# Performance work log

Measured on AMD Instinct MI355X. Metric: run time of the kernel, lower is better.

## Reference

```python
import jax, jax.numpy as jnp
import numpy as np

D_MODEL = 1024
NUM_HEADS = 16
D_K = D_MODEL // NUM_HEADS


def setup_inputs() -> dict:
    key = jax.random.key(0)
    ks = jax.random.split(key, 12)
    B, S = 2, 2048
    s = 1.0 / np.sqrt(D_MODEL)
    inp = {
        "query": jax.random.normal(ks[0], (B, S, D_MODEL), jnp.float32),
        "key": jax.random.normal(ks[1], (B, S, D_MODEL), jnp.float32),
        "value": jax.random.normal(ks[2], (B, S, D_MODEL), jnp.float32),
        "w_q": jax.random.normal(ks[3], (D_MODEL, D_MODEL), jnp.float32) * s,
        "b_q": jax.random.normal(ks[4], (D_MODEL,), jnp.float32) * 0.01,
        "w_k": jax.random.normal(ks[5], (D_MODEL, D_MODEL), jnp.float32) * s,
        "b_k": jax.random.normal(ks[6], (D_MODEL,), jnp.float32) * 0.01,
        "w_v": jax.random.normal(ks[7], (D_MODEL, D_MODEL), jnp.float32) * s,
        "b_v": jax.random.normal(ks[8], (D_MODEL,), jnp.float32) * 0.01,
        "w_o": jax.random.normal(ks[9], (D_MODEL, D_MODEL), jnp.float32) * s,
        "b_o": jax.random.normal(ks[10], (D_MODEL,), jnp.float32) * 0.01,
    }
    return inp


def _split_heads(x):
    # [B, S, d_model] -> [B, H, S, d_k]
    B, S, _ = x.shape
    return x.reshape(B, S, NUM_HEADS, D_K).transpose(0, 2, 1, 3)


def reference(query, key, value, w_q, b_q, w_k, b_k, w_v, b_v, w_o, b_o):
    B, S, _ = query.shape
    Q = _split_heads(query @ w_q.T + b_q)
    K = _split_heads(key @ w_k.T + b_k)
    V = _split_heads(value @ w_v.T + b_v)
    scale = 1.0 / jnp.sqrt(jnp.asarray(D_K, Q.dtype))
    scores = jnp.einsum("bhqd,bhkd->bhqk", Q, K) * scale  # [B,H,S,S]
    attn = jax.nn.softmax(scores, axis=-1)
    ctx = jnp.einsum("bhqk,bhkd->bhqd", attn, V)
    ctx = ctx.transpose(0, 2, 1, 3).reshape(B, S, D_MODEL)
    return ctx @ w_o.T + b_o
```

## Files before the change

### kernel.cpp

```cpp
#include <hip/hip_runtime.h>
#include <hip/hip_bf16.h>
#include <stdint.h>

#define D_MODEL 1024
#define NHEAD   16
#define DK      64
#define SEQ     2048
#define BATCH   2

using bf16 = __bf16;
typedef __bf16 bf16x8 __attribute__((ext_vector_type(8)));
typedef float  f32x4  __attribute__((ext_vector_type(4)));
typedef float  f32x16 __attribute__((ext_vector_type(16)));
typedef unsigned uintx2 __attribute__((ext_vector_type(2)));

__device__ __forceinline__ unsigned short f2bf(float x) {
  return __builtin_bit_cast(unsigned short, (__bf16)x);
}
__device__ __forceinline__ unsigned pk2bf(float a, float b) {
  return (unsigned)f2bf(a) | ((unsigned)f2bf(b) << 16);
}
__device__ __forceinline__ float uasf(unsigned x) {
  return __builtin_bit_cast(float, x);
}
__device__ __forceinline__ unsigned fasu(float x) {
  return __builtin_bit_cast(unsigned, x);
}

__device__ __forceinline__ void gld_lds16(const void* g, void* l) {
  __builtin_amdgcn_global_load_lds(
      (const __attribute__((address_space(1))) void*)g,
      (__attribute__((address_space(3))) void*)l, 16, 0, 0);
}

__device__ __forceinline__ float xhalf_sum(float x) {
  uintx2 r = __builtin_amdgcn_permlane32_swap(fasu(x), fasu(x), false, false);
  return uasf(r[0]) + uasf(r[1]);
}

#define MHA_PACK(sv, off, dst)                                           \
  {                                                                      \
    float e0 = __builtin_amdgcn_exp2f(sv[off + 0]);                      \
    float e1 = __builtin_amdgcn_exp2f(sv[off + 1]);                      \
    float e2 = __builtin_amdgcn_exp2f(sv[off + 2]);                      \
    float e3 = __builtin_amdgcn_exp2f(sv[off + 3]);                      \
    float e4 = __builtin_amdgcn_exp2f(sv[off + 4]);                      \
    float e5 = __builtin_amdgcn_exp2f(sv[off + 5]);                      \
    float e6 = __builtin_amdgcn_exp2f(sv[off + 6]);                      \
    float e7 = __builtin_amdgcn_exp2f(sv[off + 7]);                      \
    ps += ((e0 + e1) + (e2 + e3)) + ((e4 + e5) + (e6 + e7));             \
    unsigned c0 = pk2bf(e0, e1), c1 = pk2bf(e2, e3);                     \
    unsigned c2 = pk2bf(e4, e5), c3 = pk2bf(e6, e7);                     \
    uintx2 r02 = __builtin_amdgcn_permlane32_swap(c0, c2, false, false); \
    uintx2 r13 = __builtin_amdgcn_permlane32_swap(c1, c3, false, false); \
    uint4 w; w.x = r02[0]; w.y = r13[0]; w.z = r02[1]; w.w = r13[1];     \
    dst = __builtin_bit_cast(bf16x8, w);                                 \
  }

struct ConvArgs {
  const float* src[7];
  bf16* dst[7];
};

__global__ __launch_bounds__(256) void convert_f32_bf16(ConvArgs a) {
  int v = blockIdx.x * 256 + threadIdx.x;
  int seg, off;
  if (v < 3 * 1048576) { seg = v >> 20; off = v & (1048576 - 1); }
  else { int u = v - 3 * 1048576; seg = 3 + (u >> 18); off = u & (262144 - 1); }
  float4 f = ((const float4*)a.src[seg])[off];
  ushort4 o;
  o.x = f2bf(f.x); o.y = f2bf(f.y); o.z = f2bf(f.z); o.w = f2bf(f.w);
  ((ushort4*)a.dst[seg])[off] = o;
}

__device__ __forceinline__ void gemm_qkv_core(
    const bf16* __restrict__ A, const bf16* __restrict__ B,
    const float* __restrict__ bias, bf16* __restrict__ Cout,
    int mode, int bx, int by, float oscale, char* lds) {
  constexpr int BUF = 16384;
  constexpr int NKT = D_MODEL / 32;
  const int tid  = threadIdx.x;
  const int lane = tid & 63;
  const int wave = tid >> 6;
  const int wr = wave >> 1, wc = wave & 1;
  const int t = lane >> 4, q = lane & 15;

  f32x4 acc[4][4];
#pragma unroll
  for (int i = 0; i < 4; ++i)
#pragma unroll
    for (int j = 0; j < 4; ++j) acc[i][j] = (f32x4){0.f, 0.f, 0.f, 0.f};

  const char* Abase = (const char*)(A + (size_t)bx * 128 * D_MODEL);
  const char* Bbase = (const char*)(B + (size_t)by * 128 * D_MODEL);

  const char* gA[2]; char* sA[2]; const char* gB[2]; char* sB[2];
#pragma unroll
  for (int i = 0; i < 2; ++i) {
    int c = tid + i * 256, row = c >> 2;
    int src = ((c & 3) * 16) ^ ((row & 3) << 4);
    gA[i] = Abase + (size_t)row * (D_MODEL * 2) + src;
    sA[i] = lds + c * 16;
    gB[i] = Bbase + (size_t)row * (D_MODEL * 2) + src;
    sB[i] = lds + 8192 + c * 16;
  }

  const char* aA[4]; const char* aB[4];
#pragma unroll
  for (int f = 0; f < 4; ++f) {
    int ra = wr * 64 + f * 16 + q;
    aA[f] = lds + ra * 64 + ((t * 16) ^ ((q & 3) << 4));
    int rb = wc * 64 + f * 16 + q;
    aB[f] = lds + 8192 + rb * 64 + ((t * 16) ^ ((q & 3) << 4));
  }

#pragma unroll
  for (int i = 0; i < 2; ++i) { gld_lds16(gA[i], sA[i]); gld_lds16(gB[i], sB[i]); }
#pragma unroll
  for (int i = 0; i < 2; ++i) {
    gld_lds16(gA[i] + 64, sA[i] + BUF); gld_lds16(gB[i] + 64, sB[i] + BUF);
  }
  asm volatile("s_waitcnt vmcnt(4)" ::: "memory");
  __builtin_amdgcn_s_barrier();

#pragma unroll
  for (int kt = 0; kt < NKT; ++kt) {
    const int CUR = (kt % 3) * BUF;
    if (kt + 2 < NKT) {
      const int NB = ((kt + 2) % 3) * BUF;
#pragma unroll
      for (int i = 0; i < 2; ++i) {
        gld_lds16(gA[i] + (kt + 2) * 64, sA[i] + NB);
        gld_lds16(gB[i] + (kt + 2) * 64, sB[i] + NB);
      }
    }
    bf16x8 af[4], bfv[4];
#pragma unroll
    for (int f = 0; f < 4; ++f) af[f]  = *(const bf16x8*)(aA[f] + CUR);
#pragma unroll
    for (int f = 0; f < 4; ++f) bfv[f] = *(const bf16x8*)(aB[f] + CUR);
    __builtin_amdgcn_s_setprio(1);
#pragma unroll
    for (int fm = 0; fm < 4; ++fm)
#pragma unroll
      for (int fn = 0; fn < 4; ++fn)
        acc[fm][fn] = __builtin_amdgcn_mfma_f32_16x16x32_bf16(
            af[fm], bfv[fn], acc[fm][fn], 0, 0, 0);
    __builtin_amdgcn_s_setprio(0);
    if (kt + 2 < NKT)      asm volatile("s_waitcnt vmcnt(4)" ::: "memory");
    else if (kt + 1 < NKT) asm volatile("s_waitcnt vmcnt(0)" ::: "memory");
    __builtin_amdgcn_s_barrier();
  }

#pragma unroll
  for (int fm = 0; fm < 4; ++fm)
#pragma unroll
    for (int fn = 0; fn < 4; ++fn)
#pragma unroll
      for (int jj = 0; jj < 4; ++jj) {
        int m = bx * 128 + wr * 64 + fm * 16 + t * 4 + jj;
        int n = by * 128 + wc * 64 + fn * 16 + q;
        float v = acc[fm][fn][jj];
        if (mode == 0) {
          v = (v + bias[n]) * oscale;
          int b = m >> 11, s = m & (SEQ - 1), h = n >> 6, d = n & 63;
          Cout[(((size_t)(b * NHEAD + h)) * SEQ + s) * DK + d] = (bf16)v;
        } else {
          v += bias[m];
          int h = m >> 6, d = m & 63, b = n >> 11, s = n & (SEQ - 1);
          Cout[(((size_t)(b * NHEAD + h)) * DK + d) * SEQ + s] = (bf16)v;
        }
      }
}

struct QkvArgs {
  const bf16* A[3]; const bf16* B[3]; const float* bias[3]; bf16* out[3];
};

__global__ __launch_bounds__(256, 2) void gemm_qkv(QkvArgs a) {
  __shared__ char lds[3 * 16384];
  int z = blockIdx.z;
  int mode = (z == 2) ? 1 : 0;
  int bx = (z == 2) ? blockIdx.y : blockIdx.x;
  int by = (z == 2) ? blockIdx.x : blockIdx.y;
  float osc = (z == 0) ? 0.18033688011112042f : 1.0f;
  gemm_qkv_core(a.A[z], a.B[z], a.bias[z], a.out[z], mode, bx, by, osc, lds);
}

template <int BM>
__device__ __forceinline__ void gemm_core(
    const bf16* __restrict__ A, const bf16* __restrict__ B,
    const float* __restrict__ bias, float* __restrict__ Cout,
    int bx, int by, char* lds) {
  constexpr int FM   = BM / 32;
  constexpr int ACH  = BM / 32;
  constexpr int HALF = BM * 128 + 16384;
  const int tid  = threadIdx.x;
  const int lane = tid & 63;
  const int wave = tid >> 6;
  const int wr = wave >> 1, wc = wave & 1;
  const int t = lane >> 4, q = lane & 15;

  f32x4 acc[FM][4];
#pragma unroll
  for (int i = 0; i < FM; ++i)
#pragma unroll
    for (int j = 0; j < 4; ++j) acc[i][j] = (f32x4){0.f, 0.f, 0.f, 0.f};

  const char* Abase = (const char*)(A + (size_t)bx * BM * D_MODEL);
  const char* Bbase = (const char*)(B + (size_t)by * 128 * D_MODEL);

  const char* gA[ACH]; char* sA[ACH];
  const char* gB[4];   char* sB[4];
#pragma unroll
  for (int i = 0; i < ACH; ++i) {
    int c = tid + i * 256, row = c >> 3;
    int src = ((c & 7) * 16) ^ ((row & 7) << 4);
    gA[i] = Abase + (size_t)row * (D_MODEL * 2) + src;
    sA[i] = lds + c * 16;
  }
#pragma unroll
  for (int i = 0; i < 4; ++i) {
    int c = tid + i * 256, row = c >> 3;
    int src = ((c & 7) * 16) ^ ((row & 7) << 4);
    gB[i] = Bbase + (size_t)row * (D_MODEL * 2) + src;
    sB[i] = lds + BM * 128 + c * 16;
  }

  const char* aA[FM][2]; const char* aB[4][2];
#pragma unroll
  for (int f = 0; f < FM; ++f)
#pragma unroll
    for (int ks = 0; ks < 2; ++ks) {
      int ra = wr * (BM / 2) + f * 16 + q;
      aA[f][ks] = lds + ra * 128 + ((ks * 64 + t * 16) ^ ((q & 7) << 4));
    }
#pragma unroll
  for (int f = 0; f < 4; ++f)
#pragma unroll
    for (int ks = 0; ks < 2; ++ks) {
      int rb = wc * 64 + f * 16 + q;
      aB[f][ks] = lds + BM * 128 + rb * 128 + ((ks * 64 + t * 16) ^ ((q & 7) << 4));
    }

#pragma unroll
  for (int i = 0; i < ACH; ++i) gld_lds16(gA[i], sA[i]);
#pragma unroll
  for (int i = 0; i < 4; ++i)  gld_lds16(gB[i], sB[i]);
  __syncthreads();

  auto ktile = [&](int kt, int CUR) {
    if (kt + 1 < D_MODEL / 64) {
      int NXT = CUR ^ HALF;
#pragma unroll
      for (int i = 0; i < ACH; ++i) gld_lds16(gA[i] + (kt + 1) * 128, sA[i] + NXT);
#pragma unroll
      for (int i = 0; i < 4; ++i)  gld_lds16(gB[i] + (kt + 1) * 128, sB[i] + NXT);
    }
#pragma unroll
    for (int ks = 0; ks < 2; ++ks) {
      bf16x8 af[FM], bfv[4];
#pragma unroll
      for (int f = 0; f < FM; ++f) af[f] = *(const bf16x8*)(aA[f][ks] + CUR);
#pragma unroll
      for (int f = 0; f < 4; ++f)  bfv[f] = *(const bf16x8*)(aB[f][ks] + CUR);
      __builtin_amdgcn_s_setprio(1);
#pragma unroll
      for (int fm = 0; fm < FM; ++fm)
#pragma unroll
        for (int fn = 0; fn < 4; ++fn)
          acc[fm][fn] = __builtin_amdgcn_mfma_f32_16x16x32_bf16(
              af[fm], bfv[fn], acc[fm][fn], 0, 0, 0);
      __builtin_amdgcn_s_setprio(0);
    }
    __syncthreads();
  };
  for (int kt = 0; kt < D_MODEL / 64; kt += 2) {
    ktile(kt, 0);
    ktile(kt + 1, HALF);
  }

#pragma unroll
  for (int fm = 0; fm < FM; ++fm)
#pragma unroll
    for (int fn = 0; fn < 4; ++fn)
#pragma unroll
      for (int jj = 0; jj < 4; ++jj) {
        int m = bx * BM + wr * (BM / 2) + fm * 16 + t * 4 + jj;
        int n = by * 128 + wc * 64 + fn * 16 + q;
        Cout[(size_t)m * D_MODEL + n] = acc[fm][fn][jj] + bias[n];
      }
}

__global__ __launch_bounds__(256, 2) void gemm_o(
    const bf16* __restrict__ A, const bf16* __restrict__ B,
    const float* __restrict__ bias, float* __restrict__ Cout) {
  __shared__ char lds[2 * (64 * 128 + 16384)];
  gemm_core<64>(A, B, bias, Cout, blockIdx.x, blockIdx.y, lds);
}

__global__ __launch_bounds__(512, 1) void flash_attn(
    const bf16* __restrict__ Qh, const bf16* __restrict__ Kh,
    const bf16* __restrict__ Vt, bf16* __restrict__ ctx) {
  __shared__ char lds[65536];
  const int tid  = threadIdx.x;
  const int lane = tid & 63;
  const int wave = tid >> 6;
  const int lo = lane & 31;
  const int hi = lane >> 5;
  const int grp = wave >> 2;
  const int wq  = wave & 3;
  const int bh = blockIdx.x;
  const int q0 = blockIdx.y * 256 + wq * 64;

  const bf16* Qb = Qh + (size_t)bh * SEQ * DK;
  const char* Kb = (const char*)(Kh + (size_t)bh * SEQ * DK) + grp * 1024 * 128;
  const char* Vb = (const char*)(Vt + (size_t)bh * DK * SEQ) + grp * 1024 * 2;
  char* Kg = lds + grp * 16384;
  char* Vg = lds + 32768 + grp * 16384;

  bf16x8 qf0[4], qf1[4];
#pragma unroll
  for (int c = 0; c < 4; ++c) {
    qf0[c] = *(const bf16x8*)(Qb + (size_t)(q0 + lo) * DK + c * 16 + hi * 8);
    qf1[c] = *(const bf16x8*)(Qb + (size_t)(q0 + 32 + lo) * DK + c * 16 + hi * 8);
  }

  const int tg = tid & 255;
  const int srow = tg >> 3;
  const int ssrc = ((tg & 7) * 16) ^ ((srow & 7) << 4);
  const char* gK0 = Kb + (size_t)srow * 128 + ssrc;
  const char* gK1 = Kb + (size_t)(srow + 32) * 128 + ssrc;
  const char* gV0 = Vb + (size_t)srow * 4096 + ssrc;
  const char* gV1 = Vb + (size_t)(srow + 32) * 4096 + ssrc;
  char* sK0 = Kg + tg * 16;
  char* sK1 = Kg + 4096 + tg * 16;
  char* sV0 = Vg + tg * 16;
  char* sV1 = Vg + 4096 + tg * 16;

  const int key = (lo & 7) << 4;
  const char* KA[4]; const char* VA[4];
#pragma unroll
  for (int c = 0; c < 4; ++c) {
    int o = (((2 * c + hi) * 16) ^ key) + lo * 128;
    KA[c] = Kg + o;
    VA[c] = Vg + o;
  }

  f32x16 acc00 = {}, acc01 = {}, acc10 = {}, acc11 = {};
  float lsum0 = 0.f, lsum1 = 0.f;

  gld_lds16(gK0, sK0); gld_lds16(gK1, sK1);
  gld_lds16(gV0, sV0); gld_lds16(gV1, sV1);
  __syncthreads();

  auto tile = [&](int kt, int CUR) {
    if (kt + 1 < 16) {
      int nb = CUR ^ 8192;
      gld_lds16(gK0 + (kt + 1) * 8192, sK0 + nb);
      gld_lds16(gK1 + (kt + 1) * 8192, sK1 + nb);
      gld_lds16(gV0 + (kt + 1) * 128,  sV0 + nb);
      gld_lds16(gV1 + (kt + 1) * 128,  sV1 + nb);
    }

    bf16x8 pa0[4], pa1[4];
    {
      bf16x8 kf0[4], kf1[4];
#pragma unroll
      for (int c = 0; c < 4; ++c) {
        kf0[c] = *(const bf16x8*)(KA[c] + CUR);
        kf1[c] = *(const bf16x8*)(KA[c] + CUR + 4096);
      }
      f32x16 s00 = {}, s01 = {}, s10 = {}, s11 = {};
      __builtin_amdgcn_s_setprio(1);
#pragma unroll
      for (int c = 0; c < 4; ++c) {
        s00 = __builtin_amdgcn_mfma_f32_32x32x16_bf16(kf0[c], qf0[c], s00, 0, 0, 0);
        s01 = __builtin_amdgcn_mfma_f32_32x32x16_bf16(kf0[c], qf1[c], s01, 0, 0, 0);
        s10 = __builtin_amdgcn_mfma_f32_32x32x16_bf16(kf1[c], qf0[c], s10, 0, 0, 0);
        s11 = __builtin_amdgcn_mfma_f32_32x32x16_bf16(kf1[c], qf1[c], s11, 0, 0, 0);
      }
      __builtin_amdgcn_s_setprio(0);
      float ps = 0.f;
      MHA_PACK(s00, 0, pa0[0]);
      MHA_PACK(s00, 8, pa0[1]);
      MHA_PACK(s10, 0, pa0[2]);
      MHA_PACK(s10, 8, pa0[3]);
      lsum0 += ps;
      ps = 0.f;
      MHA_PACK(s01, 0, pa1[0]);
      MHA_PACK(s01, 8, pa1[1]);
      MHA_PACK(s11, 0, pa1[2]);
      MHA_PACK(s11, 8, pa1[3]);
      lsum1 += ps;
    }

    bf16x8 vf[2][4];
#pragma unroll
    for (int ks = 0; ks < 4; ++ks) {
      vf[0][ks] = *(const bf16x8*)(VA[ks] + CUR);
      vf[1][ks] = *(const bf16x8*)(VA[ks] + CUR + 4096);
    }
    __builtin_amdgcn_s_setprio(1);
#pragma unroll
    for (int ks = 0; ks < 4; ++ks) {
      acc00 = __builtin_amdgcn_mfma_f32_32x32x16_bf16(pa0[ks], vf[0][ks], acc00, 0, 0, 0);
      acc01 = __builtin_amdgcn_mfma_f32_32x32x16_bf16(pa0[ks], vf[1][ks], acc01, 0, 0, 0);
      acc10 = __builtin_amdgcn_mfma_f32_32x32x16_bf16(pa1[ks], vf[0][ks], acc10, 0, 0, 0);
      acc11 = __builtin_amdgcn_mfma_f32_32x32x16_bf16(pa1[ks], vf[1][ks], acc11, 0, 0, 0);
    }
    __builtin_amdgcn_s_setprio(0);

    __syncthreads();
  };

  for (int kt = 0; kt < 16; kt += 2) {
    tile(kt, 0);
    tile(kt + 1, 8192);
  }

  float lrun0 = xhalf_sum(lsum0);
  float lrun1 = xhalf_sum(lsum1);

  float* lsh = (float*)lds;
  float* U1  = (float*)(lds + 4096);
  if (hi == 0) {
    lsh[grp * 256 + wq * 64 + lo]      = lrun0;
    lsh[grp * 256 + wq * 64 + 32 + lo] = lrun1;
  }
  int b = bh >> 4, h = bh & 15;
#pragma unroll
  for (int qb = 0; qb < 2; ++qb) {
    const f32x16& a0 = qb ? acc10 : acc00;
    const f32x16& a1 = qb ? acc11 : acc01;
    __syncthreads();
    if (grp == 1) {
      float* dst = U1 + (size_t)(wq * 64 + lane) * 33;
#pragma unroll
      for (int r = 0; r < 16; ++r) { dst[r] = a0[r]; dst[16 + r] = a1[r]; }
    }
    __syncthreads();
    if (grp == 0) {
      const float* src = U1 + (size_t)(wq * 64 + lane) * 33;
#pragma unroll
      for (int r = 0; r < 16; ++r) {
        int row = (r & 3) + 8 * (r >> 2) + 4 * hi;
        int gr = wq * 64 + qb * 32 + row;
        float linv = 1.f / (lsh[gr] + lsh[256 + gr]);
        float o0 = (a0[r] + src[r]) * linv;
        float o1 = (a1[r] + src[16 + r]) * linv;
        int srw = q0 + qb * 32 + row;
        size_t base = ((size_t)(b * SEQ + srw)) * D_MODEL + h * 64 + lo;
        ctx[base]      = (bf16)o0;
        ctx[base + 32] = (bf16)o1;
      }
    }
  }
}

extern "C" void kernel_launch(void* const* d_in, const int* in_sizes, int n_in,
                              void* d_out, int out_size, void* d_ws, size_t ws_size,
                              hipStream_t stream) {
  const float* query = (const float*)d_in[0];
  const float* key_  = (const float*)d_in[1];
  const float* value = (const float*)d_in[2];
  const float* w_q = (const float*)d_in[3];
  const float* b_q = (const float*)d_in[4];
  const float* w_k = (const float*)d_in[5];
  const float* b_k = (const float*)d_in[6];
  const float* w_v = (const float*)d_in[7];
  const float* b_v = (const float*)d_in[8];
  const float* w_o = (const float*)d_in[9];
  const float* b_o = (const float*)d_in[10];

  char* ws = (char*)d_ws;
  const size_t MB = 1024 * 1024;
  bf16* bQ  = (bf16*)(ws + 0 * MB);
  bf16* bK  = (bf16*)(ws + 8 * MB);
  bf16* bV  = (bf16*)(ws + 16 * MB);
  bf16* bWq = (bf16*)(ws + 24 * MB);
  bf16* bWk = (bf16*)(ws + 26 * MB);
  bf16* bWv = (bf16*)(ws + 28 * MB);
  bf16* bWo = (bf16*)(ws + 30 * MB);
  bf16* Qh  = (bf16*)(ws + 32 * MB);
  bf16* Kh  = (bf16*)(ws + 40 * MB);
  bf16* Vth = (bf16*)(ws + 48 * MB);
  bf16* ctx = (bf16*)(ws + 56 * MB);

  ConvArgs ca;
  ca.src[0] = query; ca.src[1] = key_; ca.src[2] = value;
  ca.src[3] = w_q;   ca.src[4] = w_k;  ca.src[5] = w_v; ca.src[6] = w_o;
  ca.dst[0] = bQ;  ca.dst[1] = bK;  ca.dst[2] = bV;
  ca.dst[3] = bWq; ca.dst[4] = bWk; ca.dst[5] = bWv; ca.dst[6] = bWo;
  convert_f32_bf16<<<16384, 256, 0, stream>>>(ca);

  QkvArgs qa;
  qa.A[0] = bQ;  qa.B[0] = bWq; qa.bias[0] = b_q; qa.out[0] = Qh;
  qa.A[1] = bK;  qa.B[1] = bWk; qa.bias[1] = b_k; qa.out[1] = Kh;
  qa.A[2] = bWv; qa.B[2] = bV;  qa.bias[2] = b_v; qa.out[2] = Vth;
  gemm_qkv<<<dim3(32, 8, 3), 256, 0, stream>>>(qa);

  flash_attn<<<dim3(32, 8), 512, 0, stream>>>(Qh, Kh, Vth, ctx);

  gemm_o<<<dim3(64, 8), 256, 0, stream>>>(ctx, bWo, b_o, (float*)d_out);
}
```

Before: 122.8 us.

## Stage two K/V tiles per barrier in flash attention with larger LDS ring

```diff
diff --git a/kernel.cpp b/kernel.cpp
--- a/kernel.cpp
+++ b/kernel.cpp
@@ -302,7 +302,7 @@
 __global__ __launch_bounds__(512, 1) void flash_attn(
     const bf16* __restrict__ Qh, const bf16* __restrict__ Kh,
     const bf16* __restrict__ Vt, bf16* __restrict__ ctx) {
-  __shared__ char lds[65536];
+  __shared__ char lds[131072];
   const int tid  = threadIdx.x;
   const int lane = tid & 63;
   const int wave = tid >> 6;
@@ -316,8 +316,8 @@
   const bf16* Qb = Qh + (size_t)bh * SEQ * DK;
   const char* Kb = (const char*)(Kh + (size_t)bh * SEQ * DK) + grp * 1024 * 128;
   const char* Vb = (const char*)(Vt + (size_t)bh * DK * SEQ) + grp * 1024 * 2;
-  char* Kg = lds + grp * 16384;
-  char* Vg = lds + 32768 + grp * 16384;
+  char* Kg = lds + grp * 32768;
+  char* Vg = lds + 65536 + grp * 32768;
 
   bf16x8 qf0[4], qf1[4];
 #pragma unroll
@@ -350,26 +350,25 @@
   f32x16 acc00 = {}, acc01 = {}, acc10 = {}, acc11 = {};
   float lsum0 = 0.f, lsum1 = 0.f;
 
-  gld_lds16(gK0, sK0); gld_lds16(gK1, sK1);
-  gld_lds16(gV0, sV0); gld_lds16(gV1, sV1);
-  __syncthreads();
-
-  auto tile = [&](int kt, int CUR) {
-    if (kt + 1 < 16) {
-      int nb = CUR ^ 8192;
-      gld_lds16(gK0 + (kt + 1) * 8192, sK0 + nb);
-      gld_lds16(gK1 + (kt + 1) * 8192, sK1 + nb);
-      gld_lds16(gV0 + (kt + 1) * 128,  sV0 + nb);
-      gld_lds16(gV1 + (kt + 1) * 128,  sV1 + nb);
-    }
-
+  auto stage2 = [&](int t, int NXT) {
+    gld_lds16(gK0 + (size_t)t * 8192, sK0 + NXT);
+    gld_lds16(gK1 + (size_t)t * 8192, sK1 + NXT);
+    gld_lds16(gV0 + (size_t)t * 128,  sV0 + NXT);
+    gld_lds16(gV1 + (size_t)t * 128,  sV1 + NXT);
+    gld_lds16(gK0 + (size_t)(t + 1) * 8192, sK0 + NXT + 8192);
+    gld_lds16(gK1 + (size_t)(t + 1) * 8192, sK1 + NXT + 8192);
+    gld_lds16(gV0 + (size_t)(t + 1) * 128,  sV0 + NXT + 8192);
+    gld_lds16(gV1 + (size_t)(t + 1) * 128,  sV1 + NXT + 8192);
+  };
+
+  auto comp = [&](int SL) {
     bf16x8 pa0[4], pa1[4];
     {
       bf16x8 kf0[4], kf1[4];
 #pragma unroll
       for (int c = 0; c < 4; ++c) {
-        kf0[c] = *(const bf16x8*)(KA[c] + CUR);
-        kf1[c] = *(const bf16x8*)(KA[c] + CUR + 4096);
+        kf0[c] = *(const bf16x8*)(KA[c] + SL);
+        kf1[c] = *(const bf16x8*)(KA[c] + SL + 4096);
       }
       f32x16 s00 = {}, s01 = {}, s10 = {}, s11 = {};
       __builtin_amdgcn_s_setprio(1);
@@ -394,12 +393,11 @@
       MHA_PACK(s11, 8, pa1[3]);
       lsum1 += ps;
     }
-
     bf16x8 vf[2][4];
 #pragma unroll
     for (int ks = 0; ks < 4; ++ks) {
-      vf[0][ks] = *(const bf16x8*)(VA[ks] + CUR);
-      vf[1][ks] = *(const bf16x8*)(VA[ks] + CUR + 4096);
+      vf[0][ks] = *(const bf16x8*)(VA[ks] + SL);
+      vf[1][ks] = *(const bf16x8*)(VA[ks] + SL + 4096);
     }
     __builtin_amdgcn_s_setprio(1);
 #pragma unroll
@@ -410,13 +408,20 @@
       acc11 = __builtin_amdgcn_mfma_f32_32x32x16_bf16(pa1[ks], vf[1][ks], acc11, 0, 0, 0);
     }
     __builtin_amdgcn_s_setprio(0);
-
+  };
+
+  stage2(0, 0);
+  __syncthreads();
+
+  for (int p = 0; p < 8; p += 2) {
+    if (p < 7) stage2(2 * p + 2, 16384);
+    comp(0);
+    comp(8192);
     __syncthreads();
-  };
-
-  for (int kt = 0; kt < 16; kt += 2) {
-    tile(kt, 0);
-    tile(kt + 1, 8192);
+    if (p + 1 < 7) stage2(2 * p + 4, 0);
+    comp(16384);
+    comp(24576);
+    __syncthreads();
   }
 
   float lrun0 = xhalf_sum(lsum0);
```

After: 158.7 us. 29.2% more time.

## Triple-buffer K/V tiles in flash attention with prefetch distance two

Applied to the files above, without the earlier changes.

```diff
diff --git a/kernel.cpp b/kernel.cpp
--- a/kernel.cpp
+++ b/kernel.cpp
@@ -302,7 +302,7 @@
 __global__ __launch_bounds__(512, 1) void flash_attn(
     const bf16* __restrict__ Qh, const bf16* __restrict__ Kh,
     const bf16* __restrict__ Vt, bf16* __restrict__ ctx) {
-  __shared__ char lds[65536];
+  __shared__ char lds[98304];
   const int tid  = threadIdx.x;
   const int lane = tid & 63;
   const int wave = tid >> 6;
@@ -316,8 +316,7 @@
   const bf16* Qb = Qh + (size_t)bh * SEQ * DK;
   const char* Kb = (const char*)(Kh + (size_t)bh * SEQ * DK) + grp * 1024 * 128;
   const char* Vb = (const char*)(Vt + (size_t)bh * DK * SEQ) + grp * 1024 * 2;
-  char* Kg = lds + grp * 16384;
-  char* Vg = lds + 32768 + grp * 16384;
+  char* Kg = lds + grp * 49152;
 
   bf16x8 qf0[4], qf1[4];
 #pragma unroll
@@ -335,8 +334,8 @@
   const char* gV1 = Vb + (size_t)(srow + 32) * 4096 + ssrc;
   char* sK0 = Kg + tg * 16;
   char* sK1 = Kg + 4096 + tg * 16;
-  char* sV0 = Vg + tg * 16;
-  char* sV1 = Vg + 4096 + tg * 16;
+  char* sV0 = Kg + 8192 + tg * 16;
+  char* sV1 = Kg + 12288 + tg * 16;
 
   const int key = (lo & 7) << 4;
   const char* KA[4]; const char* VA[4];
@@ -344,62 +343,59 @@
   for (int c = 0; c < 4; ++c) {
     int o = (((2 * c + hi) * 16) ^ key) + lo * 128;
     KA[c] = Kg + o;
-    VA[c] = Vg + o;
+    VA[c] = Kg + 8192 + o;
   }
 
   f32x16 acc00 = {}, acc01 = {}, acc10 = {}, acc11 = {};
   float lsum0 = 0.f, lsum1 = 0.f;
 
-  gld_lds16(gK0, sK0); gld_lds16(gK1, sK1);
-  gld_lds16(gV0, sV0); gld_lds16(gV1, sV1);
-  __syncthreads();
-
-  auto tile = [&](int kt, int CUR) {
-    if (kt + 1 < 16) {
-      int nb = CUR ^ 8192;
-      gld_lds16(gK0 + (kt + 1) * 8192, sK0 + nb);
-      gld_lds16(gK1 + (kt + 1) * 8192, sK1 + nb);
-      gld_lds16(gV0 + (kt + 1) * 128,  sV0 + nb);
-      gld_lds16(gV1 + (kt + 1) * 128,  sV1 + nb);
-    }
+  auto stage = [&](int t, int SL) {
+    gld_lds16(gK0 + (size_t)t * 8192, sK0 + SL);
+    gld_lds16(gK1 + (size_t)t * 8192, sK1 + SL);
+    gld_lds16(gV0 + (size_t)t * 128,  sV0 + SL);
+    gld_lds16(gV1 + (size_t)t * 128,  sV1 + SL);
+  };
+
+  auto tile = [&](int kt, int SL, int SS) {
+    if (kt + 2 < 16) stage(kt + 2, SS);
 
     bf16x8 pa0[4], pa1[4];
     {
-      bf16x8 kf0[4], kf1[4];
+      bf16x8 kf[4];
+#pragma unroll
+      for (int c = 0; c < 4; ++c) kf[c] = *(const bf16x8*)(KA[c] + SL);
+      f32x16 s00 = {}, s01 = {};
+      __builtin_amdgcn_s_setprio(1);
 #pragma unroll
       for (int c = 0; c < 4; ++c) {
-        kf0[c] = *(const bf16x8*)(KA[c] + CUR);
-        kf1[c] = *(const bf16x8*)(KA[c] + CUR + 4096);
-      }
-      f32x16 s00 = {}, s01 = {}, s10 = {}, s11 = {};
-      __builtin_amdgcn_s_setprio(1);
-#pragma unroll
-      for (int c = 0; c < 4; ++c) {
-        s00 = __builtin_amdgcn_mfma_f32_32x32x16_bf16(kf0[c], qf0[c], s00, 0, 0, 0);
-        s01 = __builtin_amdgcn_mfma_f32_32x32x16_bf16(kf0[c], qf1[c], s01, 0, 0, 0);
-        s10 = __builtin_amdgcn_mfma_f32_32x32x16_bf16(kf1[c], qf0[c], s10, 0, 0, 0);
-        s11 = __builtin_amdgcn_mfma_f32_32x32x16_bf16(kf1[c], qf1[c], s11, 0, 0, 0);
+        s00 = __builtin_amdgcn_mfma_f32_32x32x16_bf16(kf[c], qf0[c], s00, 0, 0, 0);
+        s01 = __builtin_amdgcn_mfma_f32_32x32x16_bf16(kf[c], qf1[c], s01, 0, 0, 0);
       }
       __builtin_amdgcn_s_setprio(0);
-      float ps = 0.f;
-      MHA_PACK(s00, 0, pa0[0]);
-      MHA_PACK(s00, 8, pa0[1]);
-      MHA_PACK(s10, 0, pa0[2]);
-      MHA_PACK(s10, 8, pa0[3]);
-      lsum0 += ps;
-      ps = 0.f;
-      MHA_PACK(s01, 0, pa1[0]);
-      MHA_PACK(s01, 8, pa1[1]);
-      MHA_PACK(s11, 0, pa1[2]);
-      MHA_PACK(s11, 8, pa1[3]);
-      lsum1 += ps;
+      { float ps = 0.f; MHA_PACK(s00, 0, pa0[0]); MHA_PACK(s00, 8, pa0[1]); lsum0 += ps; }
+      { float ps = 0.f; MHA_PACK(s01, 0, pa1[0]); MHA_PACK(s01, 8, pa1[1]); lsum1 += ps; }
+    }
+    {
+      bf16x8 kf[4];
+#pragma unroll
+      for (int c = 0; c < 4; ++c) kf[c] = *(const bf16x8*)(KA[c] + SL + 4096);
+      f32x16 s10 = {}, s11 = {};
+      __builtin_amdgcn_s_setprio(1);
+#pragma unroll
+      for (int c = 0; c < 4; ++c) {
+        s10 = __builtin_amdgcn_mfma_f32_32x32x16_bf16(kf[c], qf0[c], s10, 0, 0, 0);
+        s11 = __builtin_amdgcn_mfma_f32_32x32x16_bf16(kf[c], qf1[c], s11, 0, 0, 0);
+      }
+      __builtin_amdgcn_s_setprio(0);
+      { float ps = 0.f; MHA_PACK(s10, 0, pa0[2]); MHA_PACK(s10, 8, pa0[3]); lsum0 += ps; }
+      { float ps = 0.f; MHA_PACK(s11, 0, pa1[2]); MHA_PACK(s11, 8, pa1[3]); lsum1 += ps; }
     }
 
     bf16x8 vf[2][4];
 #pragma unroll
     for (int ks = 0; ks < 4; ++ks) {
-      vf[0][ks] = *(const bf16x8*)(VA[ks] + CUR);
-      vf[1][ks] = *(const bf16x8*)(VA[ks] + CUR + 4096);
+      vf[0][ks] = *(const bf16x8*)(VA[ks] + SL);
+      vf[1][ks] = *(const bf16x8*)(VA[ks] + SL + 4096);
     }
     __builtin_amdgcn_s_setprio(1);
 #pragma unroll
@@ -411,12 +407,21 @@
     }
     __builtin_amdgcn_s_setprio(0);
 
-    __syncthreads();
+    if (kt + 2 < 16) asm volatile("s_waitcnt vmcnt(4)" ::: "memory");
+    else             asm volatile("s_waitcnt vmcnt(0)" ::: "memory");
+    __builtin_amdgcn_s_barrier();
   };
 
-  for (int kt = 0; kt < 16; kt += 2) {
-    tile(kt, 0);
-    tile(kt + 1, 8192);
+  stage(0, 0);
+  stage(1, 16384);
+  asm volatile("s_waitcnt vmcnt(4)" ::: "memory");
+  __builtin_amdgcn_s_barrier();
+
+  tile(0, 0, 32768);
+  for (int k0 = 1; k0 < 16; k0 += 3) {
+    tile(k0,     16384, 0);
+    tile(k0 + 1, 32768, 16384);
+    tile(k0 + 2, 0,     32768);
   }
 
   float lrun0 = xhalf_sum(lsum0);
```

After: 188.0 us. 53.1% more time.

## Enlarge QKV GEMM tile to 256x128 with 1D grid mapping

Applied to the files above, without the earlier changes.

```diff
diff --git a/kernel.cpp b/kernel.cpp
--- a/kernel.cpp
+++ b/kernel.cpp
@@ -77,7 +77,7 @@
     const bf16* __restrict__ A, const bf16* __restrict__ B,
     const float* __restrict__ bias, bf16* __restrict__ Cout,
     int mode, int bx, int by, float oscale, char* lds) {
-  constexpr int BUF = 16384;
+  constexpr int BUF = 24576;
   constexpr int NKT = D_MODEL / 32;
   const int tid  = threadIdx.x;
   const int lane = tid & 63;
@@ -85,80 +85,68 @@
   const int wr = wave >> 1, wc = wave & 1;
   const int t = lane >> 4, q = lane & 15;
 
-  f32x4 acc[4][4];
-#pragma unroll
-  for (int i = 0; i < 4; ++i)
+  f32x4 acc[8][4];
+#pragma unroll
+  for (int i = 0; i < 8; ++i)
 #pragma unroll
     for (int j = 0; j < 4; ++j) acc[i][j] = (f32x4){0.f, 0.f, 0.f, 0.f};
 
-  const char* Abase = (const char*)(A + (size_t)bx * 128 * D_MODEL);
+  const char* Abase = (const char*)(A + (size_t)bx * 256 * D_MODEL);
   const char* Bbase = (const char*)(B + (size_t)by * 128 * D_MODEL);
 
-  const char* gA[2]; char* sA[2]; const char* gB[2]; char* sB[2];
-#pragma unroll
-  for (int i = 0; i < 2; ++i) {
-    int c = tid + i * 256, row = c >> 2;
-    int src = ((c & 3) * 16) ^ ((row & 3) << 4);
-    gA[i] = Abase + (size_t)row * (D_MODEL * 2) + src;
-    sA[i] = lds + c * 16;
-    gB[i] = Bbase + (size_t)row * (D_MODEL * 2) + src;
-    sB[i] = lds + 8192 + c * 16;
-  }
-
-  const char* aA[4]; const char* aB[4];
-#pragma unroll
-  for (int f = 0; f < 4; ++f) {
-    int ra = wr * 64 + f * 16 + q;
-    aA[f] = lds + ra * 64 + ((t * 16) ^ ((q & 3) << 4));
-    int rb = wc * 64 + f * 16 + q;
-    aB[f] = lds + 8192 + rb * 64 + ((t * 16) ^ ((q & 3) << 4));
-  }
-
-#pragma unroll
-  for (int i = 0; i < 2; ++i) { gld_lds16(gA[i], sA[i]); gld_lds16(gB[i], sB[i]); }
-#pragma unroll
-  for (int i = 0; i < 2; ++i) {
-    gld_lds16(gA[i] + 64, sA[i] + BUF); gld_lds16(gB[i] + 64, sB[i] + BUF);
-  }
-  asm volatile("s_waitcnt vmcnt(4)" ::: "memory");
+  const int srow = tid >> 2;
+  const int ssrc = ((tid & 3) * 16) ^ ((srow & 3) << 4);
+  const char* gA0 = Abase + (size_t)srow * 2048 + ssrc;
+  const char* gB0 = Bbase + (size_t)srow * 2048 + ssrc;
+  char* sA0 = lds + tid * 16;
+  char* sB0 = lds + 16384 + tid * 16;
+
+  const char* aA0 = lds + (size_t)(wr * 128 + q) * 64 + ((t * 16) ^ ((q & 3) << 4));
+  const char* aB0 = lds + 16384 + (size_t)(wc * 64 + q) * 64 + ((t * 16) ^ ((q & 3) << 4));
+
+  auto stage = [&](int kt, int SL) {
+#pragma unroll
+    for (int i = 0; i < 4; ++i)
+      gld_lds16(gA0 + (size_t)kt * 64 + (size_t)i * 131072, sA0 + SL + i * 4096);
+#pragma unroll
+    for (int i = 0; i < 2; ++i)
+      gld_lds16(gB0 + (size_t)kt * 64 + (size_t)i * 131072, sB0 + SL + i * 4096);
+  };
+
+  stage(0, 0);
+  stage(1, BUF);
+  asm volatile("s_waitcnt vmcnt(6)" ::: "memory");
   __builtin_amdgcn_s_barrier();
 
 #pragma unroll
   for (int kt = 0; kt < NKT; ++kt) {
     const int CUR = (kt % 3) * BUF;
-    if (kt + 2 < NKT) {
-      const int NB = ((kt + 2) % 3) * BUF;
-#pragma unroll
-      for (int i = 0; i < 2; ++i) {
-        gld_lds16(gA[i] + (kt + 2) * 64, sA[i] + NB);
-        gld_lds16(gB[i] + (kt + 2) * 64, sB[i] + NB);
-      }
-    }
-    bf16x8 af[4], bfv[4];
-#pragma unroll
-    for (int f = 0; f < 4; ++f) af[f]  = *(const bf16x8*)(aA[f] + CUR);
-#pragma unroll
-    for (int f = 0; f < 4; ++f) bfv[f] = *(const bf16x8*)(aB[f] + CUR);
+    if (kt + 2 < NKT) stage(kt + 2, ((kt + 2) % 3) * BUF);
+    bf16x8 af[8], bfv[4];
+#pragma unroll
+    for (int f = 0; f < 8; ++f) af[f]  = *(const bf16x8*)(aA0 + CUR + f * 1024);
+#pragma unroll
+    for (int f = 0; f < 4; ++f) bfv[f] = *(const bf16x8*)(aB0 + CUR + f * 1024);
     __builtin_amdgcn_s_setprio(1);
 #pragma unroll
-    for (int fm = 0; fm < 4; ++fm)
+    for (int fm = 0; fm < 8; ++fm)
 #pragma unroll
       for (int fn = 0; fn < 4; ++fn)
         acc[fm][fn] = __builtin_amdgcn_mfma_f32_16x16x32_bf16(
             af[fm], bfv[fn], acc[fm][fn], 0, 0, 0);
     __builtin_amdgcn_s_setprio(0);
-    if (kt + 2 < NKT)      asm volatile("s_waitcnt vmcnt(4)" ::: "memory");
+    if (kt + 2 < NKT)      asm volatile("s_waitcnt vmcnt(6)" ::: "memory");
     else if (kt + 1 < NKT) asm volatile("s_waitcnt vmcnt(0)" ::: "memory");
     __builtin_amdgcn_s_barrier();
   }
 
 #pragma unroll
-  for (int fm = 0; fm < 4; ++fm)
+  for (int fm = 0; fm < 8; ++fm)
 #pragma unroll
     for (int fn = 0; fn < 4; ++fn)
 #pragma unroll
       for (int jj = 0; jj < 4; ++jj) {
-        int m = bx * 128 + wr * 64 + fm * 16 + t * 4 + jj;
+        int m = bx * 256 + wr * 128 + fm * 16 + t * 4 + jj;
         int n = by * 128 + wc * 64 + fn * 16 + q;
         float v = acc[fm][fn][jj];
         if (mode == 0) {
@@ -178,11 +166,13 @@
 };
 
 __global__ __launch_bounds__(256, 2) void gemm_qkv(QkvArgs a) {
-  __shared__ char lds[3 * 16384];
+  __shared__ char lds[3 * 24576];
   int z = blockIdx.z;
+  int id = blockIdx.x;
   int mode = (z == 2) ? 1 : 0;
-  int bx = (z == 2) ? blockIdx.y : blockIdx.x;
-  int by = (z == 2) ? blockIdx.x : blockIdx.y;
+  int bx, by;
+  if (z == 2) { bx = id >> 5; by = id & 31; }
+  else        { bx = id >> 3; by = id & 7;  }
   float osc = (z == 0) ? 0.18033688011112042f : 1.0f;
   gemm_qkv_core(a.A[z], a.B[z], a.bias[z], a.out[z], mode, bx, by, osc, lds);
 }
@@ -498,7 +488,7 @@
   qa.A[0] = bQ;  qa.B[0] = bWq; qa.bias[0] = b_q; qa.out[0] = Qh;
   qa.A[1] = bK;  qa.B[1] = bWk; qa.bias[1] = b_k; qa.out[1] = Kh;
   qa.A[2] = bWv; qa.B[2] = bV;  qa.bias[2] = b_v; qa.out[2] = Vth;
-  gemm_qkv<<<dim3(32, 8, 3), 256, 0, stream>>>(qa);
+  gemm_qkv<<<dim3(128, 1, 3), 256, 0, stream>>>(qa);
 
   flash_attn<<<dim3(32, 8), 512, 0, stream>>>(Qh, Kh, Vth, ctx);
 
```

Result: slower. 136.6 us (+11.2%).
